# Kernel optimization log

Measured on AMD Instinct MI355X. Metric: run time of the kernel, lower is better.

The kernel has to match this reference:

```python
import jax, jax.numpy as jnp
import numpy as np

N, E, F, H, C1 = 50000, 1_600_000, 48, 1, 16  # nodes, edges, in_feats, heads, conv out


def setup_inputs() -> dict:
    key = jax.random.key(0)
    ks = jax.random.split(key, 12)
    in_ = jax.random.normal(ks[0], (N, F), dtype=jnp.float32)
    edge_index = jax.random.randint(ks[1], (2, E), 0, N, dtype=jnp.int64)
    labels = jax.random.bernoulli(ks[2], 0.5, (N, 1)).astype(jnp.float32)
    weights = jax.random.uniform(ks[3], (N, 1), dtype=jnp.float32) + 0.5
    s = 0.1  # PyG FeaStConv init: normal(0, 0.1)
    W = jax.random.normal(ks[4], (F, H * C1), dtype=jnp.float32) * s
    u = jax.random.normal(ks[5], (F, H), dtype=jnp.float32) * s
    c = jax.random.normal(ks[6], (H,), dtype=jnp.float32) * s
    bias = jax.random.normal(ks[7], (C1,), dtype=jnp.float32) * s
    lin1_w = jax.random.normal(ks[8], (C1, 8), dtype=jnp.float32) * (1.0 / np.sqrt(C1))
    lin1_b = jnp.zeros((8,), dtype=jnp.float32)
    out_w = jax.random.normal(ks[9], (8, 1), dtype=jnp.float32) * (1.0 / np.sqrt(8))
    out_b = jnp.zeros((1,), dtype=jnp.float32)
    return {"in_": in_, "edge_index": edge_index, "labels": labels,
            "weights": weights, "W": W, "u": u, "c": c, "bias": bias,
            "lin1_w": lin1_w, "lin1_b": lin1_b, "out_w": out_w, "out_b": out_b}


def feast_conv(x, edge_index, W, u, c, bias):
    n = x.shape[0]
    loop = jnp.arange(n, dtype=edge_index.dtype)  # add_self_loops=True
    src = jnp.concatenate([edge_index[0], loop])
    dst = jnp.concatenate([edge_index[1], loop])
    xj = x[src]                                   # [E+N, F] gather
    xi = x[dst]
    q = jax.nn.softmax((xj - xi) @ u + c, axis=-1)            # [E+N, H]
    xw = (xj @ W).reshape(-1, H, C1)                           # [E+N, H, C1]
    msg = jnp.einsum('ehc,eh->ec', xw, q)                      # [E+N, C1]
    agg = jax.ops.segment_sum(msg, dst, num_segments=n)        # scatter-sum
    deg = jax.ops.segment_sum(jnp.ones_like(dst, dtype=x.dtype), dst, num_segments=n)
    return agg / jnp.maximum(deg, 1.0)[:, None] + bias         # mean aggregation


def reference(in_, edge_index, labels, weights, W, u, c, bias, lin1_w, lin1_b, out_w, out_b):
    x = jax.nn.relu(feast_conv(in_, edge_index, W, u, c, bias))
    x = jax.nn.relu(x @ lin1_w + lin1_b)
    p = jax.nn.sigmoid(x @ out_w + out_b)                      # [N, 1]
    eps = 1e-7
    pc = jnp.clip(p, eps, 1.0 - eps)
    bce = -(labels * jnp.log(pc) + (1.0 - labels) * jnp.log(1.0 - pc))
    loss = jnp.mean(weights * bce)
    return (loss, p)
```

## Files before the change

### kernel.cpp

```cpp
#include <hip/hip_runtime.h>

constexpr int N_NODES  = 50000;
constexpr int N_EDGES  = 1600000;
constexpr int F_IN     = 48;
constexpr int C1_OUT   = 16;

constexpr int BNODES    = 64;
constexpr int NBINS     = 782;
constexpr int FILL_BLKS = 256;
constexpr int EPB       = N_EDGES / FILL_BLKS;
constexpr int SCAP      = 16;
constexpr int OCAP      = 16384;
constexpr int BIN_INTS  = FILL_BLKS * SCAP;
constexpr int HNODES    = 32;
constexpr int AGG_BLKS  = NBINS * 2;
constexpr int ROWCAP    = 98;
constexpr int XW_BLKS   = 49;

constexpr size_t OFLOW_OFF = 256;
constexpr size_t XW_OFF    = OFLOW_OFF + (size_t)OCAP * 4;
constexpr size_t GSLOT_OFF = XW_OFF + (size_t)N_NODES * C1_OUT * 4;

__device__ __forceinline__ void xw_body(int n, const float* __restrict__ x,
                                        const float* __restrict__ W,
                                        float* __restrict__ xw)
{
    const float4* xr = (const float4*)(x + (long)n * F_IN);
    float h[C1_OUT];
    #pragma unroll
    for (int c = 0; c < C1_OUT; ++c) h[c] = 0.f;
    #pragma unroll
    for (int k = 0; k < F_IN / 4; ++k) {
        float4 v = xr[k];
        #pragma unroll
        for (int c = 0; c < C1_OUT; ++c) {
            h[c] = fmaf(v.x, W[(4*k+0)*C1_OUT + c],
                   fmaf(v.y, W[(4*k+1)*C1_OUT + c],
                   fmaf(v.z, W[(4*k+2)*C1_OUT + c],
                   fmaf(v.w, W[(4*k+3)*C1_OUT + c], h[c]))));
        }
    }
    float4* o = (float4*)(xw + (long)n * C1_OUT);
    o[0] = make_float4(h[0],  h[1],  h[2],  h[3]);
    o[1] = make_float4(h[4],  h[5],  h[6],  h[7]);
    o[2] = make_float4(h[8],  h[9],  h[10], h[11]);
    o[3] = make_float4(h[12], h[13], h[14], h[15]);
}

__global__ __launch_bounds__(1024)
void k_fill_xw(const int* __restrict__ src, const int* __restrict__ dst,
               int* __restrict__ gslot, int* __restrict__ ocnt,
               unsigned int* __restrict__ oflow,
               const float* __restrict__ x, const float* __restrict__ W,
               float* __restrict__ xw)
{
    __shared__ int lcnt[NBINS];
    __shared__ int lstage[NBINS * SCAP];

    if (blockIdx.x >= FILL_BLKS) {
        int n = (blockIdx.x - FILL_BLKS) * 1024 + threadIdx.x;
        if (n < N_NODES) xw_body(n, x, W, xw);
        return;
    }

    int tid = threadIdx.x;
    if (tid < NBINS) lcnt[tid] = 0;
    __syncthreads();

    int e0 = blockIdx.x * EPB;
    for (int i = tid; i < EPB; i += 1024) {
        int e = e0 + i;
        int s = src[e], d = dst[e];
        int b = d >> 6;
        int p = atomicAdd(&lcnt[b], 1);
        if (p < SCAP) {
            lstage[(b << 4) + p] = (s << 6) | (d & 63);
        } else {
            int g = atomicAdd(ocnt, 1);
            if (g < OCAP) oflow[g] = ((unsigned)s << 16) | (unsigned)d;
        }
    }
    __syncthreads();

    for (int idx = tid; idx < NBINS * SCAP; idx += 1024) {
        int b = idx >> 4, s = idx & 15;
        int v = (s < lcnt[b]) ? lstage[idx] : -1;
        gslot[((size_t)b * FILL_BLKS + blockIdx.x) * SCAP + s] = v;
    }
}

__global__ __launch_bounds__(256)
void k_agg(const int* __restrict__ gslot, int* __restrict__ ctrl,
           const unsigned int* __restrict__ oflow, const float* __restrict__ xw,
           const float* __restrict__ bias, const float* __restrict__ lin1_w,
           const float* __restrict__ lin1_b, const float* __restrict__ out_w,
           const float* __restrict__ out_b, const float* __restrict__ labels,
           const float* __restrict__ weights, float* __restrict__ out)
{
    __shared__ int ndeg[HNODES];
    __shared__ unsigned short lrow[HNODES][ROWCAP];
    __shared__ float acc[HNODES][17];
    __shared__ float sLossW[4];

    int B = blockIdx.x >> 1, H = blockIdx.x & 1;
    int tid = threadIdx.x, lane = tid & 63, w = tid >> 6;

    if (tid < HNODES) ndeg[tid] = 0;
    __syncthreads();

    const int4* sp = (const int4*)(gslot + (size_t)B * BIN_INTS);
    int4 q0 = sp[tid], q1 = sp[tid + 256], q2 = sp[tid + 512], q3 = sp[tid + 768];

    int oc = ctrl[0]; if (oc > OCAP) oc = OCAP;

    #define SC1(v) if ((v) >= 0 && ((((v) >> 5) & 1) == H)) {        \
        int ln = (v) & 31;                                           \
        int p = atomicAdd(&ndeg[ln], 1);                             \
        if (p < ROWCAP) lrow[ln][p] = (unsigned short)((unsigned)(v) >> 6); }
    SC1(q0.x); SC1(q0.y); SC1(q0.z); SC1(q0.w);
    SC1(q1.x); SC1(q1.y); SC1(q1.z); SC1(q1.w);
    SC1(q2.x); SC1(q2.y); SC1(q2.z); SC1(q2.w);
    SC1(q3.x); SC1(q3.y); SC1(q3.z); SC1(q3.w);
    #undef SC1
    for (int i = tid; i < oc; i += 256) {
        unsigned v = oflow[i];
        int d = (int)(v & 0xffffu);
        if ((d >> 6) == B && (((d >> 5) & 1) == H)) {
            int ln = d & 31;
            int p = atomicAdd(&ndeg[ln], 1);
            if (p < ROWCAP) lrow[ln][p] = (unsigned short)(v >> 16);
        }
    }
    __syncthreads();

    int rslot = lane >> 2, c4 = lane & 3;
    #pragma unroll
    for (int qd = 0; qd < 2; ++qd) {
        int base = w * 8 + qd * 4;
        int d0 = ndeg[base + 0]; if (d0 > ROWCAP) d0 = ROWCAP;
        int d1 = ndeg[base + 1]; if (d1 > ROWCAP) d1 = ROWCAP;
        int d2 = ndeg[base + 2]; if (d2 > ROWCAP) d2 = ROWCAP;
        int d3 = ndeg[base + 3]; if (d3 > ROWCAP) d3 = ROWCAP;
        int m01 = (d0 > d1) ? d0 : d1;
        int m23 = (d2 > d3) ? d2 : d3;
        int m = (m01 > m23) ? m01 : m23;
        float4 a0 = make_float4(0.f, 0.f, 0.f, 0.f);
        float4 a1 = a0, a2 = a0, a3 = a0;
        for (int j0 = 0; j0 < m; j0 += 16) {
            int j = j0 + rslot;
            if (j < d0) {
                int s = lrow[base + 0][j];
                float4 v = ((const float4*)(xw + (size_t)s * C1_OUT))[c4];
                a0.x += v.x; a0.y += v.y; a0.z += v.z; a0.w += v.w;
            }
            if (j < d1) {
                int s = lrow[base + 1][j];
                float4 v = ((const float4*)(xw + (size_t)s * C1_OUT))[c4];
                a1.x += v.x; a1.y += v.y; a1.z += v.z; a1.w += v.w;
            }
            if (j < d2) {
                int s = lrow[base + 2][j];
                float4 v = ((const float4*)(xw + (size_t)s * C1_OUT))[c4];
                a2.x += v.x; a2.y += v.y; a2.z += v.z; a2.w += v.w;
            }
            if (j < d3) {
                int s = lrow[base + 3][j];
                float4 v = ((const float4*)(xw + (size_t)s * C1_OUT))[c4];
                a3.x += v.x; a3.y += v.y; a3.z += v.z; a3.w += v.w;
            }
        }
        #pragma unroll
        for (int off = 4; off < 64; off <<= 1) {
            a0.x += __shfl_xor(a0.x, off, 64);
            a1.x += __shfl_xor(a1.x, off, 64);
            a2.x += __shfl_xor(a2.x, off, 64);
            a3.x += __shfl_xor(a3.x, off, 64);
            a0.y += __shfl_xor(a0.y, off, 64);
            a1.y += __shfl_xor(a1.y, off, 64);
            a2.y += __shfl_xor(a2.y, off, 64);
            a3.y += __shfl_xor(a3.y, off, 64);
            a0.z += __shfl_xor(a0.z, off, 64);
            a1.z += __shfl_xor(a1.z, off, 64);
            a2.z += __shfl_xor(a2.z, off, 64);
            a3.z += __shfl_xor(a3.z, off, 64);
            a0.w += __shfl_xor(a0.w, off, 64);
            a1.w += __shfl_xor(a1.w, off, 64);
            a2.w += __shfl_xor(a2.w, off, 64);
            a3.w += __shfl_xor(a3.w, off, 64);
        }
        if (lane < 16) {
            int nd = lane >> 2;
            float4 a = (nd == 0) ? a0 : (nd == 1) ? a1 : (nd == 2) ? a2 : a3;
            int c = lane & 3;
            int ln = base + nd;
            acc[ln][c * 4 + 0] = a.x;
            acc[ln][c * 4 + 1] = a.y;
            acc[ln][c * 4 + 2] = a.z;
            acc[ln][c * 4 + 3] = a.w;
        }
    }

    float lossw = 0.f;
    if (lane < 8) {
        int ln = w * 8 + lane;
        int n = B * BNODES + H * HNODES + ln;
        if (n < N_NODES) {
            int dg = ndeg[ln]; if (dg > ROWCAP) dg = ROWCAP;
            float inv = 1.f / (float)(dg + 1);
            const float4* xs4 = (const float4*)(xw + (size_t)n * C1_OUT);
            float xs[16];
            ((float4*)xs)[0] = xs4[0]; ((float4*)xs)[1] = xs4[1];
            ((float4*)xs)[2] = xs4[2]; ((float4*)xs)[3] = xs4[3];
            float h[16];
            #pragma unroll
            for (int c = 0; c < 16; ++c)
                h[c] = fmaxf(fmaf(acc[ln][c] + xs[c], inv, bias[c]), 0.f);
            float z = out_b[0];
            #pragma unroll
            for (int j = 0; j < 8; ++j) {
                float t = lin1_b[j];
                #pragma unroll
                for (int k = 0; k < 16; ++k) t = fmaf(h[k], lin1_w[k * 8 + j], t);
                z = fmaf(fmaxf(t, 0.f), out_w[j], z);
            }
            float p = 1.f / (1.f + __expf(-z));
            out[1 + n] = p;
            const float eps = 1e-7f;
            float pc = fminf(fmaxf(p, eps), 1.f - eps);
            float y  = labels[n];
            lossw = weights[n] * (-(y * __logf(pc) + (1.f - y) * __logf(1.f - pc)));
        }
    }
    lossw += __shfl_xor(lossw, 1, 64);
    lossw += __shfl_xor(lossw, 2, 64);
    lossw += __shfl_xor(lossw, 4, 64);
    if (lane == 0) sLossW[w] = lossw;
    __syncthreads();

    if (tid == 0) {
        float t = sLossW[0] + sLossW[1] + sLossW[2] + sLossW[3];
        float* loss_acc = (float*)&ctrl[2];
        atomicAdd(loss_acc, t);
        __threadfence();
        int r = atomicAdd(&ctrl[1], 1);
        if (r == AGG_BLKS - 1) {
            float total = atomicAdd(loss_acc, 0.f);
            out[0] = total / (float)N_NODES;
        }
    }
}

extern "C" void kernel_launch(void* const* d_in, const int* in_sizes, int n_in,
                              void* d_out, int out_size, void* d_ws, size_t ws_size,
                              hipStream_t stream)
{
    const float* x       = (const float*)d_in[0];
    const int*   eidx    = (const int*)  d_in[1];
    const float* labels  = (const float*)d_in[2];
    const float* weights = (const float*)d_in[3];
    const float* W       = (const float*)d_in[4];
    const float* bias    = (const float*)d_in[7];
    const float* lin1_w  = (const float*)d_in[8];
    const float* lin1_b  = (const float*)d_in[9];
    const float* out_w   = (const float*)d_in[10];
    const float* out_b   = (const float*)d_in[11];
    float* out = (float*)d_out;

    const int* src = eidx;
    const int* dst = eidx + N_EDGES;
    char* ws = (char*)d_ws;

    int*          ctrl  = (int*)ws;
    unsigned int* oflow = (unsigned int*)(ws + OFLOW_OFF);
    float*        xw    = (float*)(ws + XW_OFF);
    int*          gslot = (int*)(ws + GSLOT_OFF);

    hipMemsetAsync(ctrl, 0, 12, stream);
    k_fill_xw<<<FILL_BLKS + XW_BLKS, 1024, 0, stream>>>(
        src, dst, gslot, ctrl, oflow, x, W, xw);
    k_agg<<<AGG_BLKS, 256, 0, stream>>>(
        gslot, ctrl, oflow, xw, bias, lin1_w, lin1_b,
        out_w, out_b, labels, weights, out);
}
```

Measured before the change: 171.9 us.

## Use nontemporal loads/stores and process full 64-node bins per aggregation block

Marks the single-use streaming accesses (edge indices, input features, the gslot write and read) as nontemporal so they pollute the cache less and leave room for the reused xw rows. It also merges the two half-bin aggregation blocks into one block per 64-node bin. Each gslot bin is therefore read once instead of twice, and the per-half filtering is gone. In exchange the grid is half as large with twice the work per wave, which may lower parallelism and latency hiding on a GPU with many CUs.

Result: slower. 175.7 us (+2.2%).

```diff
diff --git a/kernel.cpp b/kernel.cpp
--- a/kernel.cpp
+++ b/kernel.cpp
@@ -12,14 +12,30 @@
 constexpr int SCAP      = 16;
 constexpr int OCAP      = 16384;
 constexpr int BIN_INTS  = FILL_BLKS * SCAP;
-constexpr int HNODES    = 32;
-constexpr int AGG_BLKS  = NBINS * 2;
 constexpr int ROWCAP    = 98;
 constexpr int XW_BLKS   = 49;
 
 constexpr size_t OFLOW_OFF = 256;
 constexpr size_t XW_OFF    = OFLOW_OFF + (size_t)OCAP * 4;
 constexpr size_t GSLOT_OFF = XW_OFF + (size_t)N_NODES * C1_OUT * 4;
+
+typedef int   vi4 __attribute__((ext_vector_type(4)));
+typedef float vf4 __attribute__((ext_vector_type(4)));
+
+__device__ __forceinline__ int4 ntload4(const int4* p) {
+    vi4 v = __builtin_nontemporal_load((const vi4*)p);
+    return make_int4(v.x, v.y, v.z, v.w);
+}
+__device__ __forceinline__ float4 ntloadf4(const float4* p) {
+    vf4 v = __builtin_nontemporal_load((const vf4*)p);
+    return make_float4(v.x, v.y, v.z, v.w);
+}
+__device__ __forceinline__ int ntloadi(const int* p) {
+    return __builtin_nontemporal_load(p);
+}
+__device__ __forceinline__ void ntstorei(int* p, int v) {
+    __builtin_nontemporal_store(v, p);
+}
 
 __device__ __forceinline__ void xw_body(int n, const float* __restrict__ x,
                                         const float* __restrict__ W,
@@ -31,7 +47,7 @@
     for (int c = 0; c < C1_OUT; ++c) h[c] = 0.f;
     #pragma unroll
     for (int k = 0; k < F_IN / 4; ++k) {
-        float4 v = xr[k];
+        float4 v = ntloadf4(&xr[k]);
         #pragma unroll
         for (int c = 0; c < C1_OUT; ++c) {
             h[c] = fmaf(v.x, W[(4*k+0)*C1_OUT + c],
@@ -70,7 +86,7 @@
     int e0 = blockIdx.x * EPB;
     for (int i = tid; i < EPB; i += 1024) {
         int e = e0 + i;
-        int s = src[e], d = dst[e];
+        int s = ntloadi(&src[e]), d = ntloadi(&dst[e]);
         int b = d >> 6;
         int p = atomicAdd(&lcnt[b], 1);
         if (p < SCAP) {
@@ -85,7 +101,7 @@
     for (int idx = tid; idx < NBINS * SCAP; idx += 1024) {
         int b = idx >> 4, s = idx & 15;
         int v = (s < lcnt[b]) ? lstage[idx] : -1;
-        gslot[((size_t)b * FILL_BLKS + blockIdx.x) * SCAP + s] = v;
+        ntstorei(&gslot[((size_t)b * FILL_BLKS + blockIdx.x) * SCAP + s], v);
     }
 }
 
@@ -97,25 +113,26 @@
            const float* __restrict__ out_b, const float* __restrict__ labels,
            const float* __restrict__ weights, float* __restrict__ out)
 {
-    __shared__ int ndeg[HNODES];
-    __shared__ unsigned short lrow[HNODES][ROWCAP];
-    __shared__ float acc[HNODES][17];
+    __shared__ int ndeg[BNODES];
+    __shared__ unsigned short lrow[BNODES][ROWCAP];
+    __shared__ float acc[BNODES][17];
     __shared__ float sLossW[4];
 
-    int B = blockIdx.x >> 1, H = blockIdx.x & 1;
-    int tid = threadIdx.x, lane = tid & 63, w = tid >> 6;
-
-    if (tid < HNODES) ndeg[tid] = 0;
+    int B = blockIdx.x, tid = threadIdx.x, lane = tid & 63, w = tid >> 6;
+
+    if (tid < BNODES) ndeg[tid] = 0;
     __syncthreads();
 
     const int4* sp = (const int4*)(gslot + (size_t)B * BIN_INTS);
-    int4 q0 = sp[tid], q1 = sp[tid + 256], q2 = sp[tid + 512], q3 = sp[tid + 768];
+    int4 q0 = ntload4(&sp[tid]);
+    int4 q1 = ntload4(&sp[tid + 256]);
+    int4 q2 = ntload4(&sp[tid + 512]);
+    int4 q3 = ntload4(&sp[tid + 768]);
 
     int oc = ctrl[0]; if (oc > OCAP) oc = OCAP;
 
-    #define SC1(v) if ((v) >= 0 && ((((v) >> 5) & 1) == H)) {        \
-        int ln = (v) & 31;                                           \
-        int p = atomicAdd(&ndeg[ln], 1);                             \
+    #define SC1(v) if ((v) >= 0) { int ln = (v) & 63;               \
+        int p = atomicAdd(&ndeg[ln], 1);                            \
         if (p < ROWCAP) lrow[ln][p] = (unsigned short)((unsigned)(v) >> 6); }
     SC1(q0.x); SC1(q0.y); SC1(q0.z); SC1(q0.w);
     SC1(q1.x); SC1(q1.y); SC1(q1.z); SC1(q1.w);
@@ -125,8 +142,8 @@
     for (int i = tid; i < oc; i += 256) {
         unsigned v = oflow[i];
         int d = (int)(v & 0xffffu);
-        if ((d >> 6) == B && (((d >> 5) & 1) == H)) {
-            int ln = d & 31;
+        if ((d >> 6) == B) {
+            int ln = d & 63;
             int p = atomicAdd(&ndeg[ln], 1);
             if (p < ROWCAP) lrow[ln][p] = (unsigned short)(v >> 16);
         }
@@ -135,8 +152,8 @@
 
     int rslot = lane >> 2, c4 = lane & 3;
     #pragma unroll
-    for (int qd = 0; qd < 2; ++qd) {
-        int base = w * 8 + qd * 4;
+    for (int qd = 0; qd < 4; ++qd) {
+        int base = w * 16 + qd * 4;
         int d0 = ndeg[base + 0]; if (d0 > ROWCAP) d0 = ROWCAP;
         int d1 = ndeg[base + 1]; if (d1 > ROWCAP) d1 = ROWCAP;
         int d2 = ndeg[base + 2]; if (d2 > ROWCAP) d2 = ROWCAP;
@@ -201,9 +218,9 @@
     }
 
     float lossw = 0.f;
-    if (lane < 8) {
-        int ln = w * 8 + lane;
-        int n = B * BNODES + H * HNODES + ln;
+    if (lane < 16) {
+        int ln = w * 16 + lane;
+        int n = B * BNODES + ln;
         if (n < N_NODES) {
             int dg = ndeg[ln]; if (dg > ROWCAP) dg = ROWCAP;
             float inv = 1.f / (float)(dg + 1);
@@ -234,6 +251,7 @@
     lossw += __shfl_xor(lossw, 1, 64);
     lossw += __shfl_xor(lossw, 2, 64);
     lossw += __shfl_xor(lossw, 4, 64);
+    lossw += __shfl_xor(lossw, 8, 64);
     if (lane == 0) sLossW[w] = lossw;
     __syncthreads();
 
@@ -243,7 +261,7 @@
         atomicAdd(loss_acc, t);
         __threadfence();
         int r = atomicAdd(&ctrl[1], 1);
-        if (r == AGG_BLKS - 1) {
+        if (r == NBINS - 1) {
             float total = atomicAdd(loss_acc, 0.f);
             out[0] = total / (float)N_NODES;
         }
@@ -278,7 +296,7 @@
     hipMemsetAsync(ctrl, 0, 12, stream);
     k_fill_xw<<<FILL_BLKS + XW_BLKS, 1024, 0, stream>>>(
         src, dst, gslot, ctrl, oflow, x, W, xw);
-    k_agg<<<AGG_BLKS, 256, 0, stream>>>(
+    k_agg<<<NBINS, 256, 0, stream>>>(
         gslot, ctrl, oflow, xw, bias, lin1_w, lin1_b,
         out_w, out_b, labels, weights, out);
 }
```
